# Performance work log

Hardware: AMD Instinct MI355X
Metric: run time of the kernel (lower is better)

## Reference

```python
import jax, jax.numpy as jnp
import numpy as np

N_NODES = 20000
N_GRAPH = 256
NODE_DIM = 128
MULS = (128, 64, 32)       # node irreps: 128x0e + 64x1o + 32x2e
HC = 32                    # hidden channels per irrep
HIDDEN_DIM = 64
N_PATH = 9                 # feasible uuw paths into 0e+1e+2e
W_NUMEL = N_PATH * HC * HC # 9216


def _tables():
    # real Clebsch-Gordan tensors built from cartesian tensor algebra,
    # normalized so that sum(C**2) = 2*l_out + 1 (component normalization)
    eps = np.zeros((3, 3, 3))
    eps[0, 1, 2] = eps[1, 2, 0] = eps[2, 0, 1] = 1.0
    eps[0, 2, 1] = eps[2, 1, 0] = eps[1, 0, 2] = -1.0
    s2, s6 = 1 / np.sqrt(2), 1 / np.sqrt(6)
    Q2 = np.zeros((5, 3, 3))  # orthonormal basis of traceless symmetric 3x3
    Q2[0, 0, 1] = Q2[0, 1, 0] = s2          # xy
    Q2[1, 1, 2] = Q2[1, 2, 1] = s2          # yz
    Q2[2, 0, 0] = Q2[2, 1, 1] = -s6; Q2[2, 2, 2] = 2 * s6  # z2
    Q2[3, 0, 2] = Q2[3, 2, 0] = s2          # xz
    Q2[4, 0, 0] = s2; Q2[4, 1, 1] = -s2     # x2-y2

    def nrm(C, l3):
        return C * np.sqrt((2 * l3 + 1) / (C ** 2).sum())

    C000 = np.ones((1, 1, 1))
    C022 = np.eye(5)[None, :, :]
    C110 = np.eye(3).reshape(3, 3, 1) / np.sqrt(3)
    C111 = eps / np.sqrt(2)
    C112 = np.transpose(Q2, (1, 2, 0))
    C202 = np.eye(5)[:, None, :]
    C220 = np.eye(5).reshape(5, 5, 1) / np.sqrt(5)
    M = np.einsum('iab,jdb->ijad', Q2, Q2)  # [5,5,3,3]
    C221 = nrm(np.einsum('cad,ijad->ijc', eps, M), 1)
    S = 0.5 * (M + np.transpose(M, (0, 1, 3, 2)))
    S = S - np.trace(S, axis1=2, axis2=3)[..., None, None] * np.eye(3) / 3.0
    C222 = nrm(np.einsum('kad,ijad->ijk', Q2, S), 2)
    # sph2cart change of basis: 9 spherical comps (0e+1e+2e) -> 3x3 cartesian
    Qc = np.zeros((3, 3, 9))
    Qc[:, :, 0] = np.eye(3) / np.sqrt(3)        # isotropic part
    Qc[:, :, 1:4] = eps / np.sqrt(2)            # antisymmetric part
    Qc[:, :, 4:9] = np.transpose(Q2, (1, 2, 0)) # symmetric traceless part
    return [C000, C022, C110, C111, C112, C202, C220, C221, C222], Qc

_CGS, _QC = _tables()


def setup_inputs() -> dict:
    key = jax.random.key(0)
    ks = jax.random.split(key, 12)
    f32 = jnp.float32
    d_sph = MULS[0] + 3 * MULS[1] + 5 * MULS[2]  # 480
    return {
        'x_scalar': jax.random.normal(ks[0], (N_NODES, NODE_DIM), f32),
        'x_spherical': jax.random.normal(ks[1], (N_NODES, d_sph), f32),
        'batch': jnp.sort(jax.random.randint(ks[2], (N_NODES,), 0, N_GRAPH)),
        'W0e': jax.random.normal(ks[3], (MULS[0], HC), f32),
        'W1o': jax.random.normal(ks[4], (MULS[1], HC), f32),
        'W2e': jax.random.normal(ks[5], (MULS[2], HC), f32),
        'Wm1': jax.random.normal(ks[6], (NODE_DIM, HIDDEN_DIM), f32) / np.sqrt(NODE_DIM),
        'bm1': jnp.zeros((HIDDEN_DIM,), f32),
        'Wm2': jax.random.normal(ks[7], (HIDDEN_DIM, W_NUMEL), f32) / np.sqrt(HIDDEN_DIM),
        'bm2': jnp.zeros((W_NUMEL,), f32),
        'P0': jax.random.normal(ks[8], (3 * HC,), f32),
        'P1': jax.random.normal(ks[9], (2 * HC,), f32),
        'P2': jax.random.normal(ks[10], (4 * HC,), f32),
    }


def reference(x_scalar, x_spherical, batch, W0e, W1o, W2e, Wm1, bm1, Wm2, bm2, P0, P1, P2):
    n = x_scalar.shape[0]
    m0, m1, m2 = MULS
    # split node features into irrep blocks
    x0 = x_spherical[:, :m0, None]                        # [N,128,1] 0e
    x1 = x_spherical[:, m0:m0 + 3 * m1].reshape(n, m1, 3) # [N,64,3]  1o
    x2 = x_spherical[:, m0 + 3 * m1:].reshape(n, m2, 5)   # [N,32,5]  2e
    # pre_lin: per-irrep channel mixing (e3nn-style 1/sqrt(fan_in))
    h = [jnp.einsum('num,uv->nvm', x, W) / np.sqrt(W.shape[0])
         for x, W in ((x0, W0e), (x1, W1o), (x2, W2e))]   # each [N,32,2l+1]
    # per-node tensor-product weights from scalar features
    w = (jax.nn.silu(x_scalar @ Wm1 + bm1) @ Wm2 + bm2).reshape(n, N_PATH, HC, HC)
    # uuw tensor product, path order matches _CGS
    paths = ((0, 0), (0, 2), (1, 1), (1, 1), (1, 1), (2, 0), (2, 2), (2, 2), (2, 2))
    inv_u = 1.0 / np.sqrt(HC)
    outs = []
    for k, (i, j) in enumerate(paths):
        C = jnp.asarray(_CGS[k], x_scalar.dtype)
        outs.append(jnp.einsum('pqr,nup,nuq,nuw->nwr', C, h[i], h[j], w[:, k]) * inv_u)
    # post_lin: combine paths of each output l into a single channel
    y0 = jnp.einsum('num,u->nm', jnp.concatenate([outs[0], outs[2], outs[6]], 1), P0) / np.sqrt(3 * HC)
    y1 = jnp.einsum('num,u->nm', jnp.concatenate([outs[3], outs[7]], 1), P1) / np.sqrt(2 * HC)
    y2 = jnp.einsum('num,u->nm', jnp.concatenate([outs[1], outs[4], outs[5], outs[8]], 1), P2) / np.sqrt(4 * HC)
    sph = jnp.concatenate([y0, y1, y2], axis=1)           # [N,9]
    cart = jnp.einsum('abi,ni->nab', jnp.asarray(_QC, sph.dtype), sph)  # [N,3,3]
    red = jax.ops.segment_sum(cart, batch, num_segments=N_GRAPH)        # [B,3,3]
    # if_trace is False (if_iso=False): roll every non-batch dim by 1
    return jnp.roll(jnp.roll(red, 1, axis=1), 1, axis=2)
```

## Files before the change

### kernel.cpp

```cpp
#include <hip/hip_runtime.h>
#include <math.h>

#define OFF_W2P 0
#define OFF_B2P 14336
#define WS_FLOATS 14560

#define SC_Y0 0.0180421959121758f
#define SC_Y2 0.015625f
#define S2f 0.70710678118654752f
#define S6f 0.40824829046386302f
#define TWOS2f 1.41421356237309505f
#define TWOS6f 0.81649658092772603f
#define ISQRT3 0.57735026918962576f
#define ISQRT5 0.44721359549995794f
#define H0SC 0.08838834764831845f
#define H1SC 0.125f
#define H2SC 0.17677669529663689f

__device__ __constant__ int KARR[7] = {0, 1, 2, 4, 5, 6, 8};

__global__ __launch_bounds__(256) void prep_kernel(
    const float* __restrict__ Wm2, const float* __restrict__ bm2,
    const float* __restrict__ P0, const float* __restrict__ P2,
    float* __restrict__ ws, float* __restrict__ out) {
  int j = blockIdx.x * 256 + threadIdx.x;
  if (j < 2304) out[j] = 0.f;

  if (j < 14336) {
    int s = j >> 11; int rem = j & 2047; int c = rem >> 5; int u = rem & 31;
    int k = KARR[s];
    const float* P;
    float sc;
    switch (s) {
      case 0: P = P0;      sc = SC_Y0; break;
      case 1: P = P2;      sc = SC_Y2; break;
      case 2: P = P0 + 32; sc = SC_Y0; break;
      case 3: P = P2 + 32; sc = SC_Y2; break;
      case 4: P = P2 + 64; sc = SC_Y2; break;
      case 5: P = P0 + 64; sc = SC_Y0; break;
      default: P = P2 + 96; sc = SC_Y2; break;
    }
    const float4* w4 = (const float4*)(Wm2 + c * 9216 + k * 1024 + u * 32);
    const float4* p4 = (const float4*)P;
    float acc = 0.f;
#pragma unroll
    for (int q = 0; q < 8; ++q) {
      float4 a = w4[q], b = p4[q];
      acc += a.x * b.x + a.y * b.y + a.z * b.z + a.w * b.w;
    }
    ws[OFF_W2P + c * 224 + s * 32 + u] = acc * sc;
  } else if (j < 14560) {
    int i = j - 14336; int s = i >> 5; int u = i & 31; int k = KARR[s];
    const float* P;
    float sc;
    switch (s) {
      case 0: P = P0;      sc = SC_Y0; break;
      case 1: P = P2;      sc = SC_Y2; break;
      case 2: P = P0 + 32; sc = SC_Y0; break;
      case 3: P = P2 + 32; sc = SC_Y2; break;
      case 4: P = P2 + 64; sc = SC_Y2; break;
      case 5: P = P0 + 64; sc = SC_Y0; break;
      default: P = P2 + 96; sc = SC_Y2; break;
    }
    const float* b = bm2 + k * 1024 + u * 32;
    float acc = 0.f;
#pragma unroll
    for (int w = 0; w < 32; ++w) acc += b[w] * P[w];
    ws[OFF_B2P + s * 32 + u] = acc * sc;
  }
}

__global__ __launch_bounds__(256) void fused_kernel(
    const float* __restrict__ xs_g, const float* __restrict__ xsph,
    const int* __restrict__ batch,
    const float* __restrict__ W0e, const float* __restrict__ W1o,
    const float* __restrict__ W2e,
    const float* __restrict__ Wm1, const float* __restrict__ bm1,
    const float* __restrict__ ws, float* __restrict__ out, const float norm2) {
  __shared__ __align__(16) char smem[50112];
  float (*xp)[484] = (float (*)[484])smem;
  float* Vb        = (float*)(smem + 30976);
  float (*xs)[132] = (float (*)[132])(smem + 30976);
  float (*hiT)[17] = (float (*)[17])(smem + 45312);
  float (*sphs)[6] = (float (*)[6])(smem + 49664);
  int* batch_s     = (int*)(smem + 50048);

  const int tid = threadIdx.x;
  const int n0 = blockIdx.x * 16;

  for (int idx = tid; idx < 1920; idx += 256) {
    const int row = idx / 120, c4 = idx % 120;
    *(float4*)&xp[row][c4 * 4] =
        *(const float4*)(xsph + (size_t)(n0 + row) * 480 + c4 * 4);
  }
  for (int idx = tid; idx < 512; idx += 256) {
    const int row = idx >> 5, c4 = idx & 31;
    *(float4*)&xs[row][c4 * 4] =
        *(const float4*)(xs_g + (n0 + row) * 128 + c4 * 4);
  }
  if (tid < 16) batch_s[tid] = batch[n0 + tid];
  __syncthreads();

  {
    const int n = tid >> 4, c0 = (tid & 15) * 4;
    float acc[4] = {0.f, 0.f, 0.f, 0.f};
#pragma unroll 4
    for (int mq = 0; mq < 32; ++mq) {
      const float4 xv = *(float4*)&xs[n][mq * 4];
      const float xa[4] = {xv.x, xv.y, xv.z, xv.w};
#pragma unroll
      for (int r = 0; r < 4; ++r) {
        const float4 w = *(const float4*)(Wm1 + (mq * 4 + r) * 64 + c0);
        acc[0] += xa[r] * w.x; acc[1] += xa[r] * w.y;
        acc[2] += xa[r] * w.z; acc[3] += xa[r] * w.w;
      }
    }
    const float4 bb = *(const float4*)(bm1 + c0);
    const float bv[4] = {bb.x, bb.y, bb.z, bb.w};
#pragma unroll
    for (int jj = 0; jj < 4; ++jj) {
      float z = acc[jj] + bv[jj];
      hiT[c0 + jj][n] = z / (1.f + __expf(-z));
    }
  }
  __syncthreads();

  if (tid < 224) {
    const int og = tid >> 3, ng = tid & 7;
    const int o0 = og * 8, n = ng * 2;
    const float4 blo = *(const float4*)(ws + OFF_B2P + o0);
    const float4 bhi = *(const float4*)(ws + OFF_B2P + o0 + 4);
    float acc[2][8];
#pragma unroll
    for (int i = 0; i < 2; ++i) {
      acc[i][0] = blo.x; acc[i][1] = blo.y; acc[i][2] = blo.z; acc[i][3] = blo.w;
      acc[i][4] = bhi.x; acc[i][5] = bhi.y; acc[i][6] = bhi.z; acc[i][7] = bhi.w;
    }
#pragma unroll 2
    for (int c = 0; c < 64; ++c) {
      const float h0v = hiT[c][n], h1v = hiT[c][n + 1];
      const float4 wlo = *(const float4*)(ws + OFF_W2P + c * 224 + o0);
      const float4 whi = *(const float4*)(ws + OFF_W2P + c * 224 + o0 + 4);
      const float wv[8] = {wlo.x, wlo.y, wlo.z, wlo.w, whi.x, whi.y, whi.z, whi.w};
#pragma unroll
      for (int jj = 0; jj < 8; ++jj) {
        acc[0][jj] += h0v * wv[jj];
        acc[1][jj] += h1v * wv[jj];
      }
    }
#pragma unroll
    for (int i = 0; i < 2; ++i) {
      float4 a = {acc[i][0], acc[i][1], acc[i][2], acc[i][3]};
      float4 b = {acc[i][4], acc[i][5], acc[i][6], acc[i][7]};
      *(float4*)&Vb[(n + i) * 224 + o0] = a;
      *(float4*)&Vb[(n + i) * 224 + o0 + 4] = b;
    }
  }
  __syncthreads();

  {
    const int n = tid >> 4, ug = tid & 15;
    const int u0 = ug * 2;
    float h0acc[2] = {0.f, 0.f};
    float h1acc[3][2] = {{0.f}};
    float h2acc[5][2] = {{0.f}};

#pragma unroll 4
    for (int mq = 0; mq < 32; ++mq) {
      const float4 xv = *(float4*)&xp[n][mq * 4];
      const float xa[4] = {xv.x, xv.y, xv.z, xv.w};
#pragma unroll
      for (int r = 0; r < 4; ++r) {
        const float2 w = *(const float2*)(W0e + (mq * 4 + r) * 32 + u0);
        h0acc[0] += xa[r] * w.x;
        h0acc[1] += xa[r] * w.y;
      }
    }
#pragma unroll 2
    for (int mq = 0; mq < 16; ++mq) {
      const float4 a0 = *(float4*)&xp[n][128 + mq * 12];
      const float4 a1 = *(float4*)&xp[n][128 + mq * 12 + 4];
      const float4 a2 = *(float4*)&xp[n][128 + mq * 12 + 8];
      const float xa[12] = {a0.x, a0.y, a0.z, a0.w, a1.x, a1.y, a1.z, a1.w,
                            a2.x, a2.y, a2.z, a2.w};
#pragma unroll
      for (int mm = 0; mm < 4; ++mm) {
        const float2 w = *(const float2*)(W1o + (mq * 4 + mm) * 32 + u0);
#pragma unroll
        for (int j = 0; j < 3; ++j) {
          h1acc[j][0] += xa[mm * 3 + j] * w.x;
          h1acc[j][1] += xa[mm * 3 + j] * w.y;
        }
      }
    }
#pragma unroll 2
    for (int mq = 0; mq < 8; ++mq) {
      const float4 a0 = *(float4*)&xp[n][320 + mq * 20];
      const float4 a1 = *(float4*)&xp[n][320 + mq * 20 + 4];
      const float4 a2 = *(float4*)&xp[n][320 + mq * 20 + 8];
      const float4 a3 = *(float4*)&xp[n][320 + mq * 20 + 12];
      const float4 a4 = *(float4*)&xp[n][320 + mq * 20 + 16];
      const float xa[20] = {a0.x, a0.y, a0.z, a0.w, a1.x, a1.y, a1.z, a1.w,
                            a2.x, a2.y, a2.z, a2.w, a3.x, a3.y, a3.z, a3.w,
                            a4.x, a4.y, a4.z, a4.w};
#pragma unroll
      for (int mm = 0; mm < 4; ++mm) {
        const float2 w = *(const float2*)(W2e + (mq * 4 + mm) * 32 + u0);
#pragma unroll
        for (int j = 0; j < 5; ++j) {
          h2acc[j][0] += xa[mm * 5 + j] * w.x;
          h2acc[j][1] += xa[mm * 5 + j] * w.y;
        }
      }
    }

    float y0s = 0.f, y2s[5] = {0.f, 0.f, 0.f, 0.f, 0.f};
    const float* Vn = Vb + n * 224 + u0;
#pragma unroll
    for (int uu = 0; uu < 2; ++uu) {
      const float h0 = h0acc[uu] * H0SC;
      const float h1a = h1acc[0][uu] * H1SC;
      const float h1b = h1acc[1][uu] * H1SC;
      const float h1c = h1acc[2][uu] * H1SC;
      float h2v[5];
#pragma unroll
      for (int j = 0; j < 5; ++j) h2v[j] = h2acc[j][uu] * H2SC;

      const float v0 = Vn[uu],       v1 = Vn[32 + uu],
                  v2 = Vn[64 + uu],  v3 = Vn[96 + uu],
                  v4 = Vn[128 + uu], v5 = Vn[160 + uu],
                  v6 = Vn[192 + uu];

      const float d11 = h1a * h1a + h1b * h1b + h1c * h1c;
      const float d22 = h2v[0] * h2v[0] + h2v[1] * h2v[1] + h2v[2] * h2v[2] +
                        h2v[3] * h2v[3] + h2v[4] * h2v[4];
      y0s += v0 * h0 * h0 + v2 * d11 * ISQRT3 + v5 * d22 * ISQRT5;

      const float o00 = h1a * h1a, o01 = h1a * h1b, o02 = h1a * h1c;
      const float o11 = h1b * h1b, o12 = h1b * h1c, o22 = h1c * h1c;
      const float t40 = TWOS2f * o01, t41 = TWOS2f * o12;
      const float t42 = S6f * (2.f * o22 - o00 - o11);
      const float t43 = TWOS2f * o02, t44 = S2f * (o00 - o11);

      const float A00 = -S6f * h2v[2] + S2f * h2v[4];
      const float A01 = S2f * h2v[0];
      const float A02 = S2f * h2v[3];
      const float A11 = -S6f * h2v[2] - S2f * h2v[4];
      const float A12 = S2f * h2v[1];
      const float A22 = TWOS6f * h2v[2];
      const float B00 = A00 * A00 + A01 * A01 + A02 * A02;
      const float B01 = A00 * A01 + A01 * A11 + A02 * A12;
      const float B02 = A00 * A02 + A01 * A12 + A02 * A22;
      const float B11 = A01 * A01 + A11 * A11 + A12 * A12;
      const float B12 = A01 * A02 + A11 * A12 + A12 * A22;
      const float B22 = A02 * A02 + A12 * A12 + A22 * A22;
      const float t80 = TWOS2f * B01, t81 = TWOS2f * B12;
      const float t82 = S6f * (2.f * B22 - B00 - B11);
      const float t83 = TWOS2f * B02, t84 = S2f * (B00 - B11);

      const float w15 = (v1 + v4) * h0;
      const float v6n = v6 * norm2;
      y2s[0] += w15 * h2v[0] + v3 * t40 + v6n * t80;
      y2s[1] += w15 * h2v[1] + v3 * t41 + v6n * t81;
      y2s[2] += w15 * h2v[2] + v3 * t42 + v6n * t82;
      y2s[3] += w15 * h2v[3] + v3 * t43 + v6n * t83;
      y2s[4] += w15 * h2v[4] + v3 * t44 + v6n * t84;
    }

#pragma unroll
    for (int off = 1; off < 16; off <<= 1) {
      y0s += __shfl_xor(y0s, off, 64);
#pragma unroll
      for (int r = 0; r < 5; ++r) y2s[r] += __shfl_xor(y2s[r], off, 64);
    }
    if (ug == 0) {
      sphs[n][0] = y0s;
#pragma unroll
      for (int r = 0; r < 5; ++r) sphs[n][1 + r] = y2s[r];
    }
  }
  __syncthreads();

  if (tid < 9) {
    const float QW[9][6] = {
        {ISQRT3, 0.f, 0.f, -S6f, 0.f, S2f},
        {0.f, S2f, 0.f, 0.f, 0.f, 0.f},
        {0.f, 0.f, 0.f, 0.f, S2f, 0.f},
        {0.f, S2f, 0.f, 0.f, 0.f, 0.f},
        {ISQRT3, 0.f, 0.f, -S6f, 0.f, -S2f},
        {0.f, 0.f, S2f, 0.f, 0.f, 0.f},
        {0.f, 0.f, 0.f, 0.f, S2f, 0.f},
        {0.f, 0.f, S2f, 0.f, 0.f, 0.f},
        {ISQRT3, 0.f, 0.f, TWOS6f, 0.f, 0.f}};
    const int a = tid / 3, b = tid % 3;
    const int rolled = ((a + 1) % 3) * 3 + ((b + 1) % 3);
    const float c0 = QW[tid][0], c1 = QW[tid][1], c2 = QW[tid][2];
    const float c3 = QW[tid][3], c4 = QW[tid][4], c5 = QW[tid][5];
    int cur_g = batch_s[0];
    float acc = 0.f;
#pragma unroll 4
    for (int q = 0; q < 16; ++q) {
      const int g = batch_s[q];
      const float val = c0 * sphs[q][0] + c1 * sphs[q][1] + c2 * sphs[q][2] +
                        c3 * sphs[q][3] + c4 * sphs[q][4] + c5 * sphs[q][5];
      if (g != cur_g) {
        atomicAdd(out + cur_g * 9 + rolled, acc);
        acc = 0.f;
        cur_g = g;
      }
      acc += val;
    }
    atomicAdd(out + cur_g * 9 + rolled, acc);
  }
}

extern "C" void kernel_launch(void* const* d_in, const int* in_sizes, int n_in,
                              void* d_out, int out_size, void* d_ws, size_t ws_size,
                              hipStream_t stream) {
  const float* x_scalar = (const float*)d_in[0];
  const float* x_sph    = (const float*)d_in[1];
  const int*   batch    = (const int*)d_in[2];
  const float* W0e      = (const float*)d_in[3];
  const float* W1o      = (const float*)d_in[4];
  const float* W2e      = (const float*)d_in[5];
  const float* Wm1      = (const float*)d_in[6];
  const float* bm1      = (const float*)d_in[7];
  const float* Wm2      = (const float*)d_in[8];
  const float* bm2      = (const float*)d_in[9];
  const float* P0       = (const float*)d_in[10];
  const float* P2       = (const float*)d_in[12];
  float* ws  = (float*)d_ws;
  float* out = (float*)d_out;

  if (ws_size < (size_t)WS_FLOATS * sizeof(float)) return;

  double Q2[5][3][3] = {};
  const double s2d = 0.70710678118654752440, s6d = 0.40824829046386301637;
  Q2[0][0][1] = Q2[0][1][0] = s2d;
  Q2[1][1][2] = Q2[1][2][1] = s2d;
  Q2[2][0][0] = Q2[2][1][1] = -s6d; Q2[2][2][2] = 2.0 * s6d;
  Q2[3][0][2] = Q2[3][2][0] = s2d;
  Q2[4][0][0] = s2d; Q2[4][1][1] = -s2d;
  double ss = 0.0;
  for (int i = 0; i < 5; ++i)
    for (int jj = 0; jj < 5; ++jj) {
      double S[3][3];
      for (int a = 0; a < 3; ++a)
        for (int d = 0; d < 3; ++d) {
          double m1 = 0, m2 = 0;
          for (int b = 0; b < 3; ++b) {
            m1 += Q2[i][a][b] * Q2[jj][d][b];
            m2 += Q2[i][d][b] * Q2[jj][a][b];
          }
          S[a][d] = 0.5 * (m1 + m2);
        }
      double tr = (S[0][0] + S[1][1] + S[2][2]) / 3.0;
      S[0][0] -= tr; S[1][1] -= tr; S[2][2] -= tr;
      for (int kk = 0; kk < 5; ++kk) {
        double cc = 0;
        for (int a = 0; a < 3; ++a)
          for (int d = 0; d < 3; ++d) cc += Q2[kk][a][d] * S[a][d];
        ss += cc * cc;
      }
    }
  const float norm2 = (float)sqrt(5.0 / ss);

  prep_kernel<<<57, 256, 0, stream>>>(Wm2, bm2, P0, P2, ws, out);
  fused_kernel<<<1250, 256, 0, stream>>>(x_scalar, x_sph, batch, W0e, W1o, W2e,
                                         Wm1, bm1, ws, out, norm2);
}
```

Before: 180.0 us.

## Split fused kernel into MLP-weight kernel and tensor-product kernel via global V buffer

Splits the single fused kernel into two. The first computes the per-node MLP-projected path weights V and writes them to a global workspace. The second loads xsph directly from global memory and computes the h0/h1/h2 projections with specialised thread groups, each thread producing 8 channels. It then combines them using V read back from global memory. This aims to cut shared memory and register pressure per kernel and to rebalance work across threads. In exchange it adds about 18 MB of global write and read traffic for V plus an extra kernel launch, and only 192 of 256 threads do projection work in that phase.

```diff
diff --git a/kernel.cpp b/kernel.cpp
--- a/kernel.cpp
+++ b/kernel.cpp
@@ -3,7 +3,8 @@
 
 #define OFF_W2P 0
 #define OFF_B2P 14336
-#define WS_FLOATS 14560
+#define OFF_V   14560
+#define WS_FLOATS 4494560
 
 #define SC_Y0 0.0180421959121758f
 #define SC_Y2 0.015625f
@@ -70,35 +71,18 @@
   }
 }
 
-__global__ __launch_bounds__(256) void fused_kernel(
-    const float* __restrict__ xs_g, const float* __restrict__ xsph,
-    const int* __restrict__ batch,
-    const float* __restrict__ W0e, const float* __restrict__ W1o,
-    const float* __restrict__ W2e,
-    const float* __restrict__ Wm1, const float* __restrict__ bm1,
-    const float* __restrict__ ws, float* __restrict__ out, const float norm2) {
-  __shared__ __align__(16) char smem[50112];
-  float (*xp)[484] = (float (*)[484])smem;
-  float* Vb        = (float*)(smem + 30976);
-  float (*xs)[132] = (float (*)[132])(smem + 30976);
-  float (*hiT)[17] = (float (*)[17])(smem + 45312);
-  float (*sphs)[6] = (float (*)[6])(smem + 49664);
-  int* batch_s     = (int*)(smem + 50048);
-
+__global__ __launch_bounds__(256) void kv_kernel(
+    const float* __restrict__ xs_g, const float* __restrict__ Wm1,
+    const float* __restrict__ bm1, float* __restrict__ ws) {
+  __shared__ __align__(16) float xs[16][132];
+  __shared__ float hiT[64][19];
   const int tid = threadIdx.x;
   const int n0 = blockIdx.x * 16;
 
-  for (int idx = tid; idx < 1920; idx += 256) {
-    const int row = idx / 120, c4 = idx % 120;
-    *(float4*)&xp[row][c4 * 4] =
-        *(const float4*)(xsph + (size_t)(n0 + row) * 480 + c4 * 4);
-  }
   for (int idx = tid; idx < 512; idx += 256) {
     const int row = idx >> 5, c4 = idx & 31;
-    *(float4*)&xs[row][c4 * 4] =
-        *(const float4*)(xs_g + (n0 + row) * 128 + c4 * 4);
-  }
-  if (tid < 16) batch_s[tid] = batch[n0 + tid];
+    *(float4*)&xs[row][c4 * 4] = *(const float4*)(xs_g + (n0 + row) * 128 + c4 * 4);
+  }
   __syncthreads();
 
   {
@@ -150,91 +134,152 @@
     }
 #pragma unroll
     for (int i = 0; i < 2; ++i) {
+      const int n_g = n0 + n + i;
       float4 a = {acc[i][0], acc[i][1], acc[i][2], acc[i][3]};
       float4 b = {acc[i][4], acc[i][5], acc[i][6], acc[i][7]};
-      *(float4*)&Vb[(n + i) * 224 + o0] = a;
-      *(float4*)&Vb[(n + i) * 224 + o0 + 4] = b;
-    }
-  }
-  __syncthreads();
-
-  {
-    const int n = tid >> 4, ug = tid & 15;
-    const int u0 = ug * 2;
-    float h0acc[2] = {0.f, 0.f};
-    float h1acc[3][2] = {{0.f}};
-    float h2acc[5][2] = {{0.f}};
-
+      *(float4*)(ws + OFF_V + n_g * 224 + o0) = a;
+      *(float4*)(ws + OFF_V + n_g * 224 + o0 + 4) = b;
+    }
+  }
+}
+
+__global__ __launch_bounds__(256) void khd_kernel(
+    const float* __restrict__ xsph, const int* __restrict__ batch,
+    const float* __restrict__ W0e, const float* __restrict__ W1o,
+    const float* __restrict__ W2e,
+    const float* __restrict__ ws, float* __restrict__ out, const float norm2) {
+  __shared__ __align__(16) char smem[33216];
+  float (*Vs)[224]     = (float (*)[224])smem;
+  float (*h0s)[32]     = (float (*)[32])(smem + 14336);
+  float (*h1s)[3][32]  = (float (*)[3][32])(smem + 16384);
+  float (*h2s)[5][32]  = (float (*)[5][32])(smem + 22528);
+  float (*sphs)[6]     = (float (*)[6])(smem + 32768);
+  int* batch_s         = (int*)(smem + 33152);
+
+  const int tid = threadIdx.x;
+  const int n0 = blockIdx.x * 16;
+
+  if (tid < 16) batch_s[tid] = batch[n0 + tid];
+
+  if (tid < 64) {
+    const int n = tid & 15, ug = tid >> 4, u0 = ug * 8;
+    const float4* x4 = (const float4*)(xsph + (size_t)(n0 + n) * 480);
+    float acc[8] = {0.f, 0.f, 0.f, 0.f, 0.f, 0.f, 0.f, 0.f};
 #pragma unroll 4
     for (int mq = 0; mq < 32; ++mq) {
-      const float4 xv = *(float4*)&xp[n][mq * 4];
+      const float4 xv = x4[mq];
       const float xa[4] = {xv.x, xv.y, xv.z, xv.w};
 #pragma unroll
       for (int r = 0; r < 4; ++r) {
-        const float2 w = *(const float2*)(W0e + (mq * 4 + r) * 32 + u0);
-        h0acc[0] += xa[r] * w.x;
-        h0acc[1] += xa[r] * w.y;
-      }
-    }
+        const float4 wl = *(const float4*)(W0e + (mq * 4 + r) * 32 + u0);
+        const float4 wh = *(const float4*)(W0e + (mq * 4 + r) * 32 + u0 + 4);
+        const float xr = xa[r];
+        acc[0] += xr * wl.x; acc[1] += xr * wl.y; acc[2] += xr * wl.z; acc[3] += xr * wl.w;
+        acc[4] += xr * wh.x; acc[5] += xr * wh.y; acc[6] += xr * wh.z; acc[7] += xr * wh.w;
+      }
+    }
+    float4 a = {acc[0] * H0SC, acc[1] * H0SC, acc[2] * H0SC, acc[3] * H0SC};
+    float4 b = {acc[4] * H0SC, acc[5] * H0SC, acc[6] * H0SC, acc[7] * H0SC};
+    *(float4*)&h0s[n][u0] = a;
+    *(float4*)&h0s[n][u0 + 4] = b;
+  } else if (tid < 128) {
+    const int t = tid - 64;
+    const int n = t & 15, ug = t >> 4, u0 = ug * 8;
+    const float4* x4 = (const float4*)(xsph + (size_t)(n0 + n) * 480);
+    float acc[3][8] = {{0.f}};
 #pragma unroll 2
     for (int mq = 0; mq < 16; ++mq) {
-      const float4 a0 = *(float4*)&xp[n][128 + mq * 12];
-      const float4 a1 = *(float4*)&xp[n][128 + mq * 12 + 4];
-      const float4 a2 = *(float4*)&xp[n][128 + mq * 12 + 8];
+      const float4 a0 = x4[32 + mq * 3];
+      const float4 a1 = x4[32 + mq * 3 + 1];
+      const float4 a2 = x4[32 + mq * 3 + 2];
       const float xa[12] = {a0.x, a0.y, a0.z, a0.w, a1.x, a1.y, a1.z, a1.w,
                             a2.x, a2.y, a2.z, a2.w};
 #pragma unroll
       for (int mm = 0; mm < 4; ++mm) {
-        const float2 w = *(const float2*)(W1o + (mq * 4 + mm) * 32 + u0);
+        const float4 wl = *(const float4*)(W1o + (mq * 4 + mm) * 32 + u0);
+        const float4 wh = *(const float4*)(W1o + (mq * 4 + mm) * 32 + u0 + 4);
+        const float wv[8] = {wl.x, wl.y, wl.z, wl.w, wh.x, wh.y, wh.z, wh.w};
 #pragma unroll
         for (int j = 0; j < 3; ++j) {
-          h1acc[j][0] += xa[mm * 3 + j] * w.x;
-          h1acc[j][1] += xa[mm * 3 + j] * w.y;
+          const float xr = xa[mm * 3 + j];
+#pragma unroll
+          for (int jj = 0; jj < 8; ++jj) acc[j][jj] += xr * wv[jj];
         }
       }
     }
+#pragma unroll
+    for (int j = 0; j < 3; ++j) {
+      float4 a = {acc[j][0] * H1SC, acc[j][1] * H1SC, acc[j][2] * H1SC, acc[j][3] * H1SC};
+      float4 b = {acc[j][4] * H1SC, acc[j][5] * H1SC, acc[j][6] * H1SC, acc[j][7] * H1SC};
+      *(float4*)&h1s[n][j][u0] = a;
+      *(float4*)&h1s[n][j][u0 + 4] = b;
+    }
+  } else if (tid < 192) {
+    const int t = tid - 128;
+    const int n = t & 15, ug = t >> 4, u0 = ug * 8;
+    const float4* x4 = (const float4*)(xsph + (size_t)(n0 + n) * 480);
+    float acc[5][8] = {{0.f}};
 #pragma unroll 2
     for (int mq = 0; mq < 8; ++mq) {
-      const float4 a0 = *(float4*)&xp[n][320 + mq * 20];
-      const float4 a1 = *(float4*)&xp[n][320 + mq * 20 + 4];
-      const float4 a2 = *(float4*)&xp[n][320 + mq * 20 + 8];
-      const float4 a3 = *(float4*)&xp[n][320 + mq * 20 + 12];
-      const float4 a4 = *(float4*)&xp[n][320 + mq * 20 + 16];
+      const float4 a0 = x4[80 + mq * 5];
+      const float4 a1 = x4[80 + mq * 5 + 1];
+      const float4 a2 = x4[80 + mq * 5 + 2];
+      const float4 a3 = x4[80 + mq * 5 + 3];
+      const float4 a4 = x4[80 + mq * 5 + 4];
       const float xa[20] = {a0.x, a0.y, a0.z, a0.w, a1.x, a1.y, a1.z, a1.w,
                             a2.x, a2.y, a2.z, a2.w, a3.x, a3.y, a3.z, a3.w,
                             a4.x, a4.y, a4.z, a4.w};
 #pragma unroll
       for (int mm = 0; mm < 4; ++mm) {
-        const float2 w = *(const float2*)(W2e + (mq * 4 + mm) * 32 + u0);
+        const float4 wl = *(const float4*)(W2e + (mq * 4 + mm) * 32 + u0);
+        const float4 wh = *(const float4*)(W2e + (mq * 4 + mm) * 32 + u0 + 4);
+        const float wv[8] = {wl.x, wl.y, wl.z, wl.w, wh.x, wh.y, wh.z, wh.w};
 #pragma unroll
         for (int j = 0; j < 5; ++j) {
-          h2acc[j][0] += xa[mm * 5 + j] * w.x;
-          h2acc[j][1] += xa[mm * 5 + j] * w.y;
+          const float xr = xa[mm * 5 + j];
+#pragma unroll
+          for (int jj = 0; jj < 8; ++jj) acc[j][jj] += xr * wv[jj];
         }
       }
     }
-
-    float y0s = 0.f, y2s[5] = {0.f, 0.f, 0.f, 0.f, 0.f};
-    const float* Vn = Vb + n * 224 + u0;
-#pragma unroll
-    for (int uu = 0; uu < 2; ++uu) {
-      const float h0 = h0acc[uu] * H0SC;
-      const float h1a = h1acc[0][uu] * H1SC;
-      const float h1b = h1acc[1][uu] * H1SC;
-      const float h1c = h1acc[2][uu] * H1SC;
+#pragma unroll
+    for (int j = 0; j < 5; ++j) {
+      float4 a = {acc[j][0] * H2SC, acc[j][1] * H2SC, acc[j][2] * H2SC, acc[j][3] * H2SC};
+      float4 b = {acc[j][4] * H2SC, acc[j][5] * H2SC, acc[j][6] * H2SC, acc[j][7] * H2SC};
+      *(float4*)&h2s[n][j][u0] = a;
+      *(float4*)&h2s[n][j][u0 + 4] = b;
+    }
+  } else {
+    const int t = tid - 192;
+    const float* Vg = ws + OFF_V + (size_t)n0 * 224;
+#pragma unroll
+    for (int q = 0; q < 14; ++q) {
+      const int idx = t + q * 64;
+      const int n = idx / 56, o4 = idx % 56;
+      *(float4*)&Vs[n][o4 * 4] = *(const float4*)(Vg + n * 224 + o4 * 4);
+    }
+  }
+  __syncthreads();
+
+  {
+    const int nl = tid >> 5, u = tid & 31;
+#pragma unroll 2
+    for (int half = 0; half < 2; ++half) {
+      const int n = half * 8 + nl;
+      const float h0 = h0s[n][u];
+      const float h1a = h1s[n][0][u], h1b = h1s[n][1][u], h1c = h1s[n][2][u];
       float h2v[5];
 #pragma unroll
-      for (int j = 0; j < 5; ++j) h2v[j] = h2acc[j][uu] * H2SC;
-
-      const float v0 = Vn[uu],       v1 = Vn[32 + uu],
-                  v2 = Vn[64 + uu],  v3 = Vn[96 + uu],
-                  v4 = Vn[128 + uu], v5 = Vn[160 + uu],
-                  v6 = Vn[192 + uu];
+      for (int j = 0; j < 5; ++j) h2v[j] = h2s[n][j][u];
+      const float v0 = Vs[n][u],       v1 = Vs[n][u + 32],
+                  v2 = Vs[n][u + 64],  v3 = Vs[n][u + 96],
+                  v4 = Vs[n][u + 128], v5 = Vs[n][u + 160],
+                  v6 = Vs[n][u + 192];
 
       const float d11 = h1a * h1a + h1b * h1b + h1c * h1c;
       const float d22 = h2v[0] * h2v[0] + h2v[1] * h2v[1] + h2v[2] * h2v[2] +
                         h2v[3] * h2v[3] + h2v[4] * h2v[4];
-      y0s += v0 * h0 * h0 + v2 * d11 * ISQRT3 + v5 * d22 * ISQRT5;
+      float y0 = v0 * h0 * h0 + v2 * d11 * ISQRT3 + v5 * d22 * ISQRT5;
 
       const float o00 = h1a * h1a, o01 = h1a * h1b, o02 = h1a * h1c;
       const float o11 = h1b * h1b, o12 = h1b * h1c, o22 = h1c * h1c;
@@ -260,23 +305,24 @@
 
       const float w15 = (v1 + v4) * h0;
       const float v6n = v6 * norm2;
-      y2s[0] += w15 * h2v[0] + v3 * t40 + v6n * t80;
-      y2s[1] += w15 * h2v[1] + v3 * t41 + v6n * t81;
-      y2s[2] += w15 * h2v[2] + v3 * t42 + v6n * t82;
-      y2s[3] += w15 * h2v[3] + v3 * t43 + v6n * t83;
-      y2s[4] += w15 * h2v[4] + v3 * t44 + v6n * t84;
-    }
-
-#pragma unroll
-    for (int off = 1; off < 16; off <<= 1) {
-      y0s += __shfl_xor(y0s, off, 64);
-#pragma unroll
-      for (int r = 0; r < 5; ++r) y2s[r] += __shfl_xor(y2s[r], off, 64);
-    }
-    if (ug == 0) {
-      sphs[n][0] = y0s;
-#pragma unroll
-      for (int r = 0; r < 5; ++r) sphs[n][1 + r] = y2s[r];
+      float y2r[5];
+      y2r[0] = w15 * h2v[0] + v3 * t40 + v6n * t80;
+      y2r[1] = w15 * h2v[1] + v3 * t41 + v6n * t81;
+      y2r[2] = w15 * h2v[2] + v3 * t42 + v6n * t82;
+      y2r[3] = w15 * h2v[3] + v3 * t43 + v6n * t83;
+      y2r[4] = w15 * h2v[4] + v3 * t44 + v6n * t84;
+
+#pragma unroll
+      for (int off = 16; off > 0; off >>= 1) {
+        y0 += __shfl_xor(y0, off, 32);
+#pragma unroll
+        for (int r = 0; r < 5; ++r) y2r[r] += __shfl_xor(y2r[r], off, 32);
+      }
+      if (u == 0) {
+        sphs[n][0] = y0;
+#pragma unroll
+        for (int r = 0; r < 5; ++r) sphs[n][1 + r] = y2r[r];
+      }
     }
   }
   __syncthreads();
@@ -366,6 +412,6 @@
   const float norm2 = (float)sqrt(5.0 / ss);
 
   prep_kernel<<<57, 256, 0, stream>>>(Wm2, bm2, P0, P2, ws, out);
-  fused_kernel<<<1250, 256, 0, stream>>>(x_scalar, x_sph, batch, W0e, W1o, W2e,
-                                         Wm1, bm1, ws, out, norm2);
+  kv_kernel<<<1250, 256, 0, stream>>>(x_scalar, Wm1, bm1, ws);
+  khd_kernel<<<1250, 256, 0, stream>>>(x_sph, batch, W0e, W1o, W2e, ws, out, norm2);
 }
```

Measured after the change: 182.6 us. About the same (+1.4%).
